# Performance work log

Hardware: AMD Instinct MI355X
Metric: run time of the kernel (lower is better)

Reference implementation:

```python
import jax, jax.numpy as jnp
import numpy as np

D_MODEL = 1024
N_HEADS = 16
HEAD_DIM = D_MODEL // N_HEADS
B, S = 4, 2048


def setup_inputs() -> dict:
    key = jax.random.key(0)
    ks = jax.random.split(key, 9)
    sd = 1.0 / np.sqrt(D_MODEL)
    x = jax.random.normal(ks[0], (B, S, D_MODEL), dtype=jnp.float32)
    wq = jax.random.uniform(ks[1], (D_MODEL, D_MODEL), jnp.float32, -sd, sd)
    bq = jax.random.uniform(ks[2], (D_MODEL,), jnp.float32, -sd, sd)
    wk = jax.random.uniform(ks[3], (HEAD_DIM, D_MODEL), jnp.float32, -sd, sd)
    bk = jax.random.uniform(ks[4], (HEAD_DIM,), jnp.float32, -sd, sd)
    wv = jax.random.uniform(ks[5], (HEAD_DIM, D_MODEL), jnp.float32, -sd, sd)
    bv = jax.random.uniform(ks[6], (HEAD_DIM,), jnp.float32, -sd, sd)
    wo = jax.random.uniform(ks[7], (D_MODEL, D_MODEL), jnp.float32, -sd, sd)
    bo = jax.random.uniform(ks[8], (D_MODEL,), jnp.float32, -sd, sd)
    return {"x": x, "wq": wq, "bq": bq, "wk": wk, "bk": bk,
            "wv": wv, "bv": bv, "wo": wo, "bo": bo}


def reference(x, wq, bq, wk, bk, wv, bv, wo, bo):
    b, s, _ = x.shape
    scale = HEAD_DIM ** -0.5
    # projections (torch Linear: x @ W.T + b)
    q = (x @ wq.T + bq).reshape(b, s, N_HEADS, HEAD_DIM)  # [B,S,H,Dh]
    k = x @ wk.T + bk  # [B,S,Dh] single shared KV head
    v = x @ wv.T + bv  # [B,S,Dh]
    # QK^T with broadcast K: [B,H,S,S]
    attn = jnp.einsum('bqhd,bkd->bhqk', q, k) * scale
    attn = jax.nn.softmax(attn, axis=-1)
    # attend with broadcast V: [B,H,S,Dh]
    out = jnp.einsum('bhqk,bkd->bqhd', attn, v).reshape(b, s, D_MODEL)
    return out @ wo.T + bo
```

## Files before the change

kernel.cpp:

```cpp
#include <hip/hip_runtime.h>
#include <hip/hip_bf16.h>

#define D_MODEL 1024
#define HEAD_DIM 64
#define N_HEADS 16
#define BATCH 4
#define SEQ 2048
#define M_TOK (BATCH * SEQ)
#define N_QKV 1152

typedef unsigned short u16;
typedef unsigned int u32;
typedef __attribute__((ext_vector_type(8))) short s8;
typedef __attribute__((ext_vector_type(4))) float f4;
typedef __attribute__((ext_vector_type(16))) float f16x;

#define SCALE_LOG2E 0.18033688011112042f

__device__ __forceinline__ u16 f2bf(float f) {
    union { float f; unsigned u; } x; x.f = f;
    unsigned r = x.u + 0x7fffu + ((x.u >> 16) & 1u);
    return (u16)(r >> 16);
}

__device__ __forceinline__ u32 cvt_pk_bf16(float lo, float hi) {
    u32 r;
    asm("v_cvt_pk_bf16_f32 %0, %1, %2" : "=v"(r) : "v"(lo), "v"(hi));
    return r;
}

__global__ void cast_bf16(const float* __restrict__ in, u16* __restrict__ out, int n4) {
    int i = blockIdx.x * 256 + threadIdx.x;
    if (i < n4) {
        float4 v = reinterpret_cast<const float4*>(in)[i];
        ushort4 o;
        o.x = f2bf(v.x); o.y = f2bf(v.y); o.z = f2bf(v.z); o.w = f2bf(v.w);
        reinterpret_cast<ushort4*>(out)[i] = o;
    }
}

__global__ void cast_wcat(const float* __restrict__ wq, const float* __restrict__ wk,
                          const float* __restrict__ wv, u16* __restrict__ wcat) {
    int row = blockIdx.x, t = threadIdx.x;
    const float* src = (row < 1024) ? wq + (size_t)row * 1024
                     : (row < 1088) ? wk + (size_t)(row - 1024) * 1024
                                    : wv + (size_t)(row - 1088) * 1024;
    float4 v = reinterpret_cast<const float4*>(src)[t];
    ushort4 o;
    o.x = f2bf(v.x); o.y = f2bf(v.y); o.z = f2bf(v.z); o.w = f2bf(v.w);
    reinterpret_cast<ushort4*>(wcat + (size_t)row * 1024)[t] = o;
}

template<int MODE>
__global__ __launch_bounds__(256, 2)
void gemm_mfma_bt(const u16* __restrict__ A, const u16* __restrict__ B,
                  const float* __restrict__ bias0,
                  const float* __restrict__ bk_, const float* __restrict__ bv_,
                  void* __restrict__ C0, u16* __restrict__ kbf,
                  u16* __restrict__ vtb, int M, int N, int K)
{
    __shared__ u16 As[128 * 64];
    __shared__ u16 Bs[128 * 64];
    const int t = threadIdx.x;
    const int lane = t & 63, wid = t >> 6;
    const int lr = lane & 15, lg = lane >> 4;
    const int wm = wid >> 1, wn = wid & 1;
    const int bm = blockIdx.y * 128, bn = blockIdx.x * 128;

    f4 acc[4][4];
#pragma unroll
    for (int i = 0; i < 4; ++i)
#pragma unroll
        for (int j = 0; j < 4; ++j) acc[i][j] = (f4){0.f, 0.f, 0.f, 0.f};

    int srow[4], sseg[4], sdst[4];
#pragma unroll
    for (int i = 0; i < 4; ++i) {
        int c = t + i * 256;
        srow[i] = c >> 3; sseg[i] = c & 7;
        sdst[i] = srow[i] * 128 + ((sseg[i] * 16) ^ ((srow[i] & 7) << 4));
    }

    const int NT = K >> 6;
    s8 pa[4], pb[4];
#pragma unroll
    for (int i = 0; i < 4; ++i) {
        pa[i] = *(const s8*)(A + (size_t)(bm + srow[i]) * K + sseg[i] * 8);
        pb[i] = *(const s8*)(B + (size_t)(bn + srow[i]) * K + sseg[i] * 8);
    }

    for (int kt = 0; kt < NT; ++kt) {
        __syncthreads();
#pragma unroll
        for (int i = 0; i < 4; ++i) {
            *(s8*)((char*)As + sdst[i]) = pa[i];
            *(s8*)((char*)Bs + sdst[i]) = pb[i];
        }
        __syncthreads();
        if (kt + 1 < NT) {
            int k0 = (kt + 1) << 6;
#pragma unroll
            for (int i = 0; i < 4; ++i) {
                pa[i] = *(const s8*)(A + (size_t)(bm + srow[i]) * K + k0 + sseg[i] * 8);
                pb[i] = *(const s8*)(B + (size_t)(bn + srow[i]) * K + k0 + sseg[i] * 8);
            }
        }
#pragma unroll
        for (int kbk = 0; kbk < 2; ++kbk) {
            s8 af[4];
#pragma unroll
            for (int rb = 0; rb < 4; ++rb) {
                int row = wm * 64 + rb * 16 + lr;
                af[rb] = *(const s8*)((const char*)As + row * 128 +
                                      ((kbk * 64 + lg * 16) ^ ((row & 7) << 4)));
            }
#pragma unroll
            for (int cb = 0; cb < 4; ++cb) {
                int rowb = wn * 64 + cb * 16 + lr;
                s8 bf = *(const s8*)((const char*)Bs + rowb * 128 +
                                     ((kbk * 64 + lg * 16) ^ ((rowb & 7) << 4)));
#pragma unroll
                for (int rb = 0; rb < 4; ++rb)
                    acc[rb][cb] = __builtin_amdgcn_mfma_f32_16x16x32_bf16(
                        af[rb], bf, acc[rb][cb], 0, 0, 0);
            }
        }
    }

#pragma unroll
    for (int cb = 0; cb < 4; ++cb) {
        int col = bn + wn * 64 + cb * 16 + lr;
        float bb;
        if (MODE == 0) bb = bias0[col];
        else bb = (col < 1024) ? bias0[col]
                : (col < 1088) ? bk_[col - 1024] : bv_[col - 1088];
#pragma unroll
        for (int rb = 0; rb < 4; ++rb)
#pragma unroll
            for (int r = 0; r < 4; ++r) {
                int row = bm + wm * 64 + rb * 16 + lg * 4 + r;
                float v = acc[rb][cb][r] + bb;
                if (MODE == 0) {
                    ((float*)C0)[(size_t)row * 1024 + col] = v;
                } else {
                    if (col < 1024)
                        ((u16*)C0)[(size_t)row * 1024 + col] = f2bf(v * SCALE_LOG2E);
                    else if (col < 1088)
                        kbf[(size_t)row * HEAD_DIM + (col - 1024)] = f2bf(v);
                    else
                        vtb[((size_t)(row >> 11) * 64 + (col - 1088)) * SEQ +
                            (row & 2047)] = f2bf(v);
                }
            }
    }
}

__global__ __launch_bounds__(256, 4)
void mqa_flash_mfma(const u16* __restrict__ qb, const u16* __restrict__ kbuf,
                    const u16* __restrict__ vtb, u16* __restrict__ ob)
{
    __shared__ u16 Ks[64 * 64];
    __shared__ u16 Vts[64 * 64];
    const int t = threadIdx.x, lane = t & 63, wid = t >> 6;
    const int l31 = lane & 31, hi = lane >> 5;
    const int qt = blockIdx.x, h = blockIdx.y, b = blockIdx.z;
    const int q0 = qt * 128 + wid * 32;

    const u16* qbase = qb + (size_t)b * SEQ * D_MODEL + h * HEAD_DIM;
    const u16* kbase = kbuf + (size_t)b * SEQ * HEAD_DIM;
    const u16* vbase = vtb + (size_t)b * HEAD_DIM * SEQ;

    s8 qf[4];
#pragma unroll
    for (int s = 0; s < 4; ++s)
        qf[s] = *(const s8*)(qbase + (size_t)(q0 + l31) * D_MODEL + s * 16 + hi * 8);

    s8 ones;
#pragma unroll
    for (int j = 0; j < 8; ++j) ones[j] = (short)0x3F80;

    f16x oacc[2], oaccS;
#pragma unroll
    for (int r = 0; r < 16; ++r) { oacc[0][r] = 0.f; oacc[1][r] = 0.f; oaccS[r] = 0.f; }

    const int c0 = t, c1 = t + 256;
    const int r0 = c0 >> 3, s0 = c0 & 7, r1 = c1 >> 3, s1 = c1 & 7;
    const int d0 = r0 * 128 + ((s0 * 16) ^ ((r0 & 7) << 4));
    const int d1 = r1 * 128 + ((s1 * 16) ^ ((r1 & 7) << 4));

    s8 pk0 = *(const s8*)(kbase + (size_t)r0 * HEAD_DIM + s0 * 8);
    s8 pk1 = *(const s8*)(kbase + (size_t)r1 * HEAD_DIM + s1 * 8);
    s8 pv0 = *(const s8*)(vbase + (size_t)r0 * SEQ + s0 * 8);
    s8 pv1 = *(const s8*)(vbase + (size_t)r1 * SEQ + s1 * 8);

    const int swz = (l31 & 7) << 4;

    for (int kt = 0; kt < SEQ / 64; ++kt) {
        __syncthreads();
        *(s8*)((char*)Ks + d0) = pk0;  *(s8*)((char*)Ks + d1) = pk1;
        *(s8*)((char*)Vts + d0) = pv0; *(s8*)((char*)Vts + d1) = pv1;
        __syncthreads();
        if (kt + 1 < SEQ / 64) {
            int kt0 = (kt + 1) * 64;
            pk0 = *(const s8*)(kbase + (size_t)(kt0 + r0) * HEAD_DIM + s0 * 8);
            pk1 = *(const s8*)(kbase + (size_t)(kt0 + r1) * HEAD_DIM + s1 * 8);
            pv0 = *(const s8*)(vbase + (size_t)r0 * SEQ + kt0 + s0 * 8);
            pv1 = *(const s8*)(vbase + (size_t)r1 * SEQ + kt0 + s1 * 8);
        }

        f16x st[2];
#pragma unroll
        for (int kb = 0; kb < 2; ++kb) {
#pragma unroll
            for (int r = 0; r < 16; ++r) st[kb][r] = 0.f;
#pragma unroll
            for (int s = 0; s < 4; ++s) {
                s8 kf = *(const s8*)((const char*)Ks + (kb * 32 + l31) * 128 +
                                     ((s * 32 + hi * 16) ^ swz));
                st[kb] = __builtin_amdgcn_mfma_f32_32x32x16_bf16(
                    kf, qf[s], st[kb], 0, 0, 0);
            }
        }

        u32 pw[4][4];
#pragma unroll
        for (int kb = 0; kb < 2; ++kb)
#pragma unroll
            for (int sub = 0; sub < 2; ++sub) {
                float c[8];
#pragma unroll
                for (int i = 0; i < 8; ++i)
                    c[i] = exp2f(st[kb][sub * 8 + i]);
                u32 A = cvt_pk_bf16(c[0], c[1]);
                u32 B = cvt_pk_bf16(c[2], c[3]);
                u32 C = cvt_pk_bf16(c[4], c[5]);
                u32 D = cvt_pk_bf16(c[6], c[7]);
                asm("v_permlane32_swap_b32 %0, %1" : "+v"(A), "+v"(C));
                asm("v_permlane32_swap_b32 %0, %1" : "+v"(B), "+v"(D));
                int s = kb * 2 + sub;
                pw[s][0] = A; pw[s][1] = B; pw[s][2] = C; pw[s][3] = D;
            }

#pragma unroll
        for (int s = 0; s < 4; ++s) {
            s8 paf = *(const s8*)&pw[s][0];
#pragma unroll
            for (int dh = 0; dh < 2; ++dh) {
                s8 vf = *(const s8*)((const char*)Vts + (dh * 32 + l31) * 128 +
                                     ((s * 32 + hi * 16) ^ swz));
                oacc[dh] = __builtin_amdgcn_mfma_f32_32x32x16_bf16(
                    paf, vf, oacc[dh], 0, 0, 0);
            }
            oaccS = __builtin_amdgcn_mfma_f32_32x32x16_bf16(
                paf, ones, oaccS, 0, 0, 0);
        }
    }

    u16* obase = ob + (size_t)b * SEQ * D_MODEL + h * HEAD_DIM;
#pragma unroll
    for (int r = 0; r < 16; ++r) {
        float inv = 1.f / oaccS[r];
        int qrow = (r & 3) + 8 * (r >> 2) + 4 * hi;
        int row = q0 + qrow;
#pragma unroll
        for (int dh = 0; dh < 2; ++dh)
            obase[(size_t)row * D_MODEL + dh * 32 + l31] =
                f2bf(oacc[dh][r] * inv);
    }
}

extern "C" void kernel_launch(void* const* d_in, const int* in_sizes, int n_in,
                              void* d_out, int out_size, void* d_ws, size_t ws_size,
                              hipStream_t stream)
{
    const float* x  = (const float*)d_in[0];
    const float* wq = (const float*)d_in[1];
    const float* bq = (const float*)d_in[2];
    const float* wk = (const float*)d_in[3];
    const float* bk = (const float*)d_in[4];
    const float* wv = (const float*)d_in[5];
    const float* bv = (const float*)d_in[6];
    const float* wo = (const float*)d_in[7];
    const float* bo = (const float*)d_in[8];
    float* out = (float*)d_out;

    u16* base = (u16*)d_ws;
    u16* xbf  = base;
    u16* qbuf = xbf  + (size_t)M_TOK * D_MODEL;
    u16* abuf = qbuf + (size_t)M_TOK * D_MODEL;
    u16* kbf  = abuf + (size_t)M_TOK * D_MODEL;
    u16* vtb  = kbf  + (size_t)M_TOK * HEAD_DIM;
    u16* wcat = vtb  + (size_t)M_TOK * HEAD_DIM;
    u16* wob  = wcat + (size_t)N_QKV * D_MODEL;

    cast_bf16<<<(M_TOK * D_MODEL / 4 + 255) / 256, 256, 0, stream>>>(
        x, xbf, M_TOK * D_MODEL / 4);
    cast_wcat<<<N_QKV, 256, 0, stream>>>(wq, wk, wv, wcat);
    cast_bf16<<<(D_MODEL * D_MODEL / 4 + 255) / 256, 256, 0, stream>>>(
        wo, wob, D_MODEL * D_MODEL / 4);

    gemm_mfma_bt<1><<<dim3(N_QKV / 128, M_TOK / 128), 256, 0, stream>>>(
        xbf, wcat, bq, bk, bv, qbuf, kbf, vtb, M_TOK, N_QKV, D_MODEL);

    mqa_flash_mfma<<<dim3(SEQ / 128, N_HEADS, BATCH), 256, 0, stream>>>(
        qbuf, kbf, vtb, abuf);

    gemm_mfma_bt<0><<<dim3(D_MODEL / 128, M_TOK / 128), 256, 0, stream>>>(
        abuf, wob, bo, nullptr, nullptr, out, nullptr, nullptr,
        M_TOK, D_MODEL, D_MODEL);
}
```

Before: 175.7 us.

## Use direct global-to-LDS loads with double-buffered shared memory in GEMM and attention

Replaces the register-staged global loads and LDS stores in both the projection GEMM and the flash-attention kernel with global_load_lds async copies into double-buffered shared tiles. The XOR swizzle moves from the LDS destination to the global source address. This removes the register round trip and one barrier per iteration, so the next tile's loads can overlap the current tile's MFMA work. It doubles LDS use, which may lower occupancy, and correctness depends on the global_load_lds lane-to-LDS layout and on the barrier waiting for the async loads.

```diff
diff --git a/kernel.cpp b/kernel.cpp
--- a/kernel.cpp
+++ b/kernel.cpp
@@ -16,6 +16,11 @@
 typedef __attribute__((ext_vector_type(16))) float f16x;
 
 #define SCALE_LOG2E 0.18033688011112042f
+
+#define GLDS(gp, lp)                                                          \
+    __builtin_amdgcn_global_load_lds(                                         \
+        (const __attribute__((address_space(1))) unsigned int*)(gp),          \
+        (__attribute__((address_space(3))) unsigned int*)(lp), 16, 0, 0)
 
 __device__ __forceinline__ u16 f2bf(float f) {
     union { float f; unsigned u; } x; x.f = f;
@@ -59,8 +64,8 @@
                   void* __restrict__ C0, u16* __restrict__ kbf,
                   u16* __restrict__ vtb, int M, int N, int K)
 {
-    __shared__ u16 As[128 * 64];
-    __shared__ u16 Bs[128 * 64];
+    __shared__ u16 As[2][128 * 64];
+    __shared__ u16 Bs[2][128 * 64];
     const int t = threadIdx.x;
     const int lane = t & 63, wid = t >> 6;
     const int lr = lane & 15, lg = lane >> 4;
@@ -73,51 +78,47 @@
 #pragma unroll
         for (int j = 0; j < 4; ++j) acc[i][j] = (f4){0.f, 0.f, 0.f, 0.f};
 
-    int srow[4], sseg[4], sdst[4];
+    int grow[4], gseg[4], lofs[4];
 #pragma unroll
     for (int i = 0; i < 4; ++i) {
         int c = t + i * 256;
-        srow[i] = c >> 3; sseg[i] = c & 7;
-        sdst[i] = srow[i] * 128 + ((sseg[i] * 16) ^ ((srow[i] & 7) << 4));
+        grow[i] = c >> 3;
+        gseg[i] = (c & 7) ^ (grow[i] & 7);
+        lofs[i] = i * 2048 + wid * 512;
     }
 
     const int NT = K >> 6;
-    s8 pa[4], pb[4];
-#pragma unroll
-    for (int i = 0; i < 4; ++i) {
-        pa[i] = *(const s8*)(A + (size_t)(bm + srow[i]) * K + sseg[i] * 8);
-        pb[i] = *(const s8*)(B + (size_t)(bn + srow[i]) * K + sseg[i] * 8);
-    }
-
+
+#define GSTAGE(bufi, k0)                                                      \
+    {                                                                         \
+        _Pragma("unroll")                                                     \
+        for (int i = 0; i < 4; ++i) {                                         \
+            GLDS(A + (size_t)(bm + grow[i]) * K + (k0) + gseg[i] * 8,         \
+                 &As[bufi][lofs[i]]);                                         \
+            GLDS(B + (size_t)(bn + grow[i]) * K + (k0) + gseg[i] * 8,         \
+                 &Bs[bufi][lofs[i]]);                                         \
+        }                                                                     \
+    }
+
+    GSTAGE(0, 0);
+    __syncthreads();
+
+    int buf = 0;
     for (int kt = 0; kt < NT; ++kt) {
-        __syncthreads();
-#pragma unroll
-        for (int i = 0; i < 4; ++i) {
-            *(s8*)((char*)As + sdst[i]) = pa[i];
-            *(s8*)((char*)Bs + sdst[i]) = pb[i];
-        }
-        __syncthreads();
-        if (kt + 1 < NT) {
-            int k0 = (kt + 1) << 6;
-#pragma unroll
-            for (int i = 0; i < 4; ++i) {
-                pa[i] = *(const s8*)(A + (size_t)(bm + srow[i]) * K + k0 + sseg[i] * 8);
-                pb[i] = *(const s8*)(B + (size_t)(bn + srow[i]) * K + k0 + sseg[i] * 8);
-            }
-        }
+        if (kt + 1 < NT) GSTAGE(buf ^ 1, (kt + 1) << 6);
 #pragma unroll
         for (int kbk = 0; kbk < 2; ++kbk) {
             s8 af[4];
 #pragma unroll
             for (int rb = 0; rb < 4; ++rb) {
                 int row = wm * 64 + rb * 16 + lr;
-                af[rb] = *(const s8*)((const char*)As + row * 128 +
+                af[rb] = *(const s8*)((const char*)As[buf] + row * 128 +
                                       ((kbk * 64 + lg * 16) ^ ((row & 7) << 4)));
             }
 #pragma unroll
             for (int cb = 0; cb < 4; ++cb) {
                 int rowb = wn * 64 + cb * 16 + lr;
-                s8 bf = *(const s8*)((const char*)Bs + rowb * 128 +
+                s8 bf = *(const s8*)((const char*)Bs[buf] + rowb * 128 +
                                      ((kbk * 64 + lg * 16) ^ ((rowb & 7) << 4)));
 #pragma unroll
                 for (int rb = 0; rb < 4; ++rb)
@@ -125,7 +126,10 @@
                         af[rb], bf, acc[rb][cb], 0, 0, 0);
             }
         }
-    }
+        __syncthreads();
+        buf ^= 1;
+    }
+#undef GSTAGE
 
 #pragma unroll
     for (int cb = 0; cb < 4; ++cb) {
@@ -159,8 +163,8 @@
 void mqa_flash_mfma(const u16* __restrict__ qb, const u16* __restrict__ kbuf,
                     const u16* __restrict__ vtb, u16* __restrict__ ob)
 {
-    __shared__ u16 Ks[64 * 64];
-    __shared__ u16 Vts[64 * 64];
+    __shared__ u16 Ks[2][64 * 64];
+    __shared__ u16 Vts[2][64 * 64];
     const int t = threadIdx.x, lane = t & 63, wid = t >> 6;
     const int l31 = lane & 31, hi = lane >> 5;
     const int qt = blockIdx.x, h = blockIdx.y, b = blockIdx.z;
@@ -170,6 +174,22 @@
     const u16* kbase = kbuf + (size_t)b * SEQ * HEAD_DIM;
     const u16* vbase = vtb + (size_t)b * HEAD_DIM * SEQ;
 
+    const int cA = t, cB = t + 256;
+    const int rA = cA >> 3, sA = (cA & 7) ^ (rA & 7);
+    const int rB = cB >> 3, sB = (cB & 7) ^ (rB & 7);
+    const int loA = wid * 512;
+    const int loB = 2048 + wid * 512;
+
+#define ASTAGE(bufi, kt0)                                                     \
+    {                                                                         \
+        GLDS(kbase + (size_t)((kt0) + rA) * HEAD_DIM + sA * 8, &Ks[bufi][loA]);\
+        GLDS(kbase + (size_t)((kt0) + rB) * HEAD_DIM + sB * 8, &Ks[bufi][loB]);\
+        GLDS(vbase + (size_t)rA * SEQ + (kt0) + sA * 8, &Vts[bufi][loA]);     \
+        GLDS(vbase + (size_t)rB * SEQ + (kt0) + sB * 8, &Vts[bufi][loB]);     \
+    }
+
+    ASTAGE(0, 0);
+
     s8 qf[4];
 #pragma unroll
     for (int s = 0; s < 4; ++s)
@@ -183,30 +203,13 @@
 #pragma unroll
     for (int r = 0; r < 16; ++r) { oacc[0][r] = 0.f; oacc[1][r] = 0.f; oaccS[r] = 0.f; }
 
-    const int c0 = t, c1 = t + 256;
-    const int r0 = c0 >> 3, s0 = c0 & 7, r1 = c1 >> 3, s1 = c1 & 7;
-    const int d0 = r0 * 128 + ((s0 * 16) ^ ((r0 & 7) << 4));
-    const int d1 = r1 * 128 + ((s1 * 16) ^ ((r1 & 7) << 4));
-
-    s8 pk0 = *(const s8*)(kbase + (size_t)r0 * HEAD_DIM + s0 * 8);
-    s8 pk1 = *(const s8*)(kbase + (size_t)r1 * HEAD_DIM + s1 * 8);
-    s8 pv0 = *(const s8*)(vbase + (size_t)r0 * SEQ + s0 * 8);
-    s8 pv1 = *(const s8*)(vbase + (size_t)r1 * SEQ + s1 * 8);
-
     const int swz = (l31 & 7) << 4;
 
+    __syncthreads();
+
+    int buf = 0;
     for (int kt = 0; kt < SEQ / 64; ++kt) {
-        __syncthreads();
-        *(s8*)((char*)Ks + d0) = pk0;  *(s8*)((char*)Ks + d1) = pk1;
-        *(s8*)((char*)Vts + d0) = pv0; *(s8*)((char*)Vts + d1) = pv1;
-        __syncthreads();
-        if (kt + 1 < SEQ / 64) {
-            int kt0 = (kt + 1) * 64;
-            pk0 = *(const s8*)(kbase + (size_t)(kt0 + r0) * HEAD_DIM + s0 * 8);
-            pk1 = *(const s8*)(kbase + (size_t)(kt0 + r1) * HEAD_DIM + s1 * 8);
-            pv0 = *(const s8*)(vbase + (size_t)r0 * SEQ + kt0 + s0 * 8);
-            pv1 = *(const s8*)(vbase + (size_t)r1 * SEQ + kt0 + s1 * 8);
-        }
+        if (kt + 1 < SEQ / 64) ASTAGE(buf ^ 1, (kt + 1) * 64);
 
         f16x st[2];
 #pragma unroll
@@ -215,7 +218,7 @@
             for (int r = 0; r < 16; ++r) st[kb][r] = 0.f;
 #pragma unroll
             for (int s = 0; s < 4; ++s) {
-                s8 kf = *(const s8*)((const char*)Ks + (kb * 32 + l31) * 128 +
+                s8 kf = *(const s8*)((const char*)Ks[buf] + (kb * 32 + l31) * 128 +
                                      ((s * 32 + hi * 16) ^ swz));
                 st[kb] = __builtin_amdgcn_mfma_f32_32x32x16_bf16(
                     kf, qf[s], st[kb], 0, 0, 0);
@@ -246,7 +249,7 @@
             s8 paf = *(const s8*)&pw[s][0];
 #pragma unroll
             for (int dh = 0; dh < 2; ++dh) {
-                s8 vf = *(const s8*)((const char*)Vts + (dh * 32 + l31) * 128 +
+                s8 vf = *(const s8*)((const char*)Vts[buf] + (dh * 32 + l31) * 128 +
                                      ((s * 32 + hi * 16) ^ swz));
                 oacc[dh] = __builtin_amdgcn_mfma_f32_32x32x16_bf16(
                     paf, vf, oacc[dh], 0, 0, 0);
@@ -254,7 +257,11 @@
             oaccS = __builtin_amdgcn_mfma_f32_32x32x16_bf16(
                 paf, ones, oaccS, 0, 0, 0);
         }
-    }
+
+        __syncthreads();
+        buf ^= 1;
+    }
+#undef ASTAGE
 
     u16* obase = ob + (size_t)b * SEQ * D_MODEL + h * HEAD_DIM;
 #pragma unroll
```

Measured after the change: 187.8 us. 6.9% more time.
